# Kernel optimization log

Hardware: AMD Instinct MI355X
Metric: run time of the kernel (lower is better)

The kernel has to match this reference:

```python
import jax, jax.numpy as jnp
import numpy as np

B, D, E, N = 2048, 4096, 512, 8192
BN_EPS = 1e-5
COS_EPS = 1e-8


def setup_inputs() -> dict:
    key = jax.random.key(0)
    k1, k2, k3, k4, k5 = jax.random.split(key, 5)
    vf = jax.random.normal(k1, (B, D), dtype=jnp.float32)
    p_wfs = jax.random.normal(k2, (B, D), dtype=jnp.float32)
    n_wfs = jax.random.normal(k3, (N, E), dtype=jnp.float32)
    # BatchNorm1d(4096) affine params (default init gamma=1, beta=0; use random-ish gamma for generality)
    gamma = jnp.ones((D,), dtype=jnp.float32)
    beta = jnp.zeros((D,), dtype=jnp.float32)
    # Linear(D -> E)
    lim = 1.0 / np.sqrt(D)
    W = jax.random.uniform(k4, (E, D), dtype=jnp.float32, minval=-lim, maxval=lim)
    b = jax.random.uniform(k5, (E,), dtype=jnp.float32, minval=-lim, maxval=lim)
    return {"vf": vf, "p_wfs": p_wfs, "n_wfs": n_wfs, "gamma": gamma, "beta": beta, "W": W, "b": b}


def _row_normalize(x, eps=COS_EPS):
    nrm = jnp.sqrt(jnp.sum(x * x, axis=-1, keepdims=True))
    return x / jnp.maximum(nrm, eps)


def reference(vf, p_wfs, n_wfs, gamma, beta, W, b):
    # BatchNorm1d in training mode: batch mean / biased variance over the batch dim
    mean = jnp.mean(vf, axis=0)
    var = jnp.mean((vf - mean) ** 2, axis=0)
    vfn = (vf - mean) * (gamma / jnp.sqrt(var + BN_EPS)) + beta  # [B, D]

    # Linear + ReLU embedding
    emb = jax.nn.relu(vfn @ W.T + b)  # [B, E]

    # p_e: row-wise cosine(normed vf, p_wfs) -> [B]
    p_e = jnp.sum(_row_normalize(vfn) * _row_normalize(p_wfs), axis=-1)

    # n_e: cosine(emb[v], n_wfs[n]) for all v,n -> one normalized GEMM [B, N]
    n_e = _row_normalize(emb) @ _row_normalize(n_wfs).T

    n_neg = n_wfs.shape[0]
    n_e_stack = n_e.reshape(-1, 1)                      # [B*N, 1]
    p_e_stack = jnp.repeat(p_e, n_neg).reshape(-1, 1)   # [B*N, 1], p_e[v] repeated N times
    return (n_e_stack, p_e_stack)
```

## Files before the change

### kernel.cpp

```cpp
#include <hip/hip_runtime.h>
#include <stdint.h>
#include <stddef.h>

#define B_ 2048
#define D_ 4096
#define E_ 512
#define N_ 8192

typedef unsigned short ushort_t;
typedef __attribute__((ext_vector_type(8))) short short8;
typedef __attribute__((ext_vector_type(4))) float floatx4;
typedef __attribute__((ext_vector_type(4))) unsigned short ushort4_t;

__device__ __forceinline__ void async_load16(const void* g, void* l) {
  __builtin_amdgcn_global_load_lds((__attribute__((address_space(1))) void*)(g),
                                   (__attribute__((address_space(3))) void*)(l), 16, 0, 0);
}

__device__ __forceinline__ ushort_t f2bf(float f) {
  unsigned int u = __float_as_uint(f);
  unsigned int r = (u + 0x7fffu + ((u >> 16) & 1u)) >> 16;
  return (ushort_t)r;
}
__device__ __forceinline__ float bf2f(ushort_t h) {
  return __uint_as_float(((unsigned int)h) << 16);
}

__global__ void bn_partial(const float* __restrict__ vf,
                           float* __restrict__ psum, float* __restrict__ psq) {
  int d = blockIdx.x * 256 + threadIdx.x;
  int chunk = blockIdx.y;
  float s = 0.f, q = 0.f;
  int r0 = chunk * 64;
  for (int r = r0; r < r0 + 64; ++r) {
    float v = vf[(size_t)r * D_ + d];
    s += v; q += v * v;
  }
  psum[chunk * D_ + d] = s;
  psq[chunk * D_ + d]  = q;
}

__global__ void bn_finalize(const float* __restrict__ psum, const float* __restrict__ psq,
                            const float* __restrict__ gamma, const float* __restrict__ beta,
                            float* __restrict__ scale, float* __restrict__ shift) {
  int d = blockIdx.x * 256 + threadIdx.x;
  float s = 0.f, q = 0.f;
  for (int c = 0; c < 32; ++c) { s += psum[c * D_ + d]; q += psq[c * D_ + d]; }
  float mean = s * (1.0f / B_);
  float var  = q * (1.0f / B_) - mean * mean;
  float sc = gamma[d] * rsqrtf(var + 1e-5f);
  scale[d] = sc;
  shift[d] = beta[d] - mean * sc;
}

__global__ void pe_kernel(const float* __restrict__ vf, const float* __restrict__ p,
                          const float* __restrict__ scale, const float* __restrict__ shift,
                          float* __restrict__ pe) {
  int v = blockIdx.x;
  const floatx4* vf4 = (const floatx4*)(vf + (size_t)v * D_);
  const floatx4* p4  = (const floatx4*)(p  + (size_t)v * D_);
  const floatx4* sc4 = (const floatx4*)scale;
  const floatx4* sh4 = (const floatx4*)shift;
  float sd = 0.f, sa = 0.f, sb = 0.f;
  for (int i = threadIdx.x; i < D_ / 4; i += 256) {
    floatx4 x = vf4[i], y = p4[i], s = sc4[i], t = sh4[i];
#pragma unroll
    for (int j = 0; j < 4; ++j) {
      float xn = x[j] * s[j] + t[j];
      sd += xn * y[j]; sa += xn * xn; sb += y[j] * y[j];
    }
  }
  for (int off = 32; off; off >>= 1) {
    sd += __shfl_down(sd, off); sa += __shfl_down(sa, off); sb += __shfl_down(sb, off);
  }
  __shared__ float red[3][4];
  int w = threadIdx.x >> 6, l = threadIdx.x & 63;
  if (l == 0) { red[0][w] = sd; red[1][w] = sa; red[2][w] = sb; }
  __syncthreads();
  if (threadIdx.x == 0) {
    sd = red[0][0] + red[0][1] + red[0][2] + red[0][3];
    sa = red[1][0] + red[1][1] + red[1][2] + red[1][3];
    sb = red[2][0] + red[2][1] + red[2][2] + red[2][3];
    float na = fmaxf(sqrtf(sa), 1e-8f), nb = fmaxf(sqrtf(sb), 1e-8f);
    pe[v] = sd / (na * nb);
  }
}

__global__ void cast_vfn(const float* __restrict__ vf, const float* __restrict__ scale,
                         const float* __restrict__ shift, ushort_t* __restrict__ out) {
  size_t i = ((size_t)blockIdx.x * 256 + threadIdx.x) * 4;
  int d = (int)(i & (D_ - 1));
  floatx4 x = *(const floatx4*)(vf + i);
  floatx4 s = *(const floatx4*)(scale + d);
  floatx4 t = *(const floatx4*)(shift + d);
  ushort4_t o;
#pragma unroll
  for (int j = 0; j < 4; ++j) o[j] = f2bf(x[j] * s[j] + t[j]);
  *(ushort4_t*)(out + i) = o;
}

__global__ void cast_w(const float* __restrict__ W, ushort_t* __restrict__ out) {
  size_t i = ((size_t)blockIdx.x * 256 + threadIdx.x) * 4;
  floatx4 x = *(const floatx4*)(W + i);
  ushort4_t o;
#pragma unroll
  for (int j = 0; j < 4; ++j) o[j] = f2bf(x[j]);
  *(ushort4_t*)(out + i) = o;
}

__global__ void nw_kernel(const float* __restrict__ nw, ushort_t* __restrict__ nwb,
                          float* __restrict__ inv_nw) {
  int n = blockIdx.x;
  int t = threadIdx.x;
  floatx4 x = ((const floatx4*)(nw + (size_t)n * E_))[t];
  float s = x[0]*x[0] + x[1]*x[1] + x[2]*x[2] + x[3]*x[3];
  ushort4_t o;
#pragma unroll
  for (int j = 0; j < 4; ++j) o[j] = f2bf(x[j]);
  ((ushort4_t*)(nwb + (size_t)n * E_))[t] = o;
  for (int off = 32; off; off >>= 1) s += __shfl_down(s, off);
  __shared__ float r2[2];
  if ((t & 63) == 0) r2[t >> 6] = s;
  __syncthreads();
  if (t == 0) inv_nw[n] = 1.f / fmaxf(sqrtf(r2[0] + r2[1]), 1e-8f);
}

__global__ void emb_norm(const ushort_t* __restrict__ emb, float* __restrict__ inv_emb) {
  int v = blockIdx.x;
  int t = threadIdx.x;
  ushort4_t x = ((const ushort4_t*)(emb + (size_t)v * E_))[t];
  float s = 0.f;
#pragma unroll
  for (int j = 0; j < 4; ++j) { float f = bf2f(x[j]); s += f * f; }
  for (int off = 32; off; off >>= 1) s += __shfl_down(s, off);
  __shared__ float r2[2];
  if ((t & 63) == 0) r2[t >> 6] = s;
  __syncthreads();
  if (t == 0) inv_emb[v] = 1.f / fmaxf(sqrtf(r2[0] + r2[1]), 1e-8f);
}

template <int BM, int BN, int BK, int WROWS, int WCOLS, int MT, int NT>
__device__ __forceinline__ void gemm_core(const ushort_t* __restrict__ A,
                                          const ushort_t* __restrict__ Bt, int K,
                                          int bm0, int bn0,
                                          ushort_t* As, ushort_t* Bs,
                                          floatx4 (&acc)[MT][NT]) {
  const int tid = threadIdx.x, w = tid >> 6, l = tid & 63;
  constexpr int ISS = BM * BK / 2048;
  const int wr = w / WCOLS, wc = w % WCOLS;
  const int m16 = l & 15, q = l >> 4;

  for (int k0 = 0; k0 < K; k0 += BK) {
#pragma unroll
    for (int i = 0; i < ISS; ++i) {
      int e = i * 2048 + tid * 8;
      int row = e / BK, col = e % BK;
      async_load16(A + (size_t)(bm0 + row) * K + (k0 + col), &As[i * 2048 + w * 512]);
    }
#pragma unroll
    for (int i = 0; i < ISS; ++i) {
      int e = i * 2048 + tid * 8;
      int row = e / BK, col = e % BK;
      async_load16(Bt + (size_t)(bn0 + row) * K + (k0 + col), &Bs[i * 2048 + w * 512]);
    }
    __syncthreads();
#pragma unroll
    for (int kc = 0; kc < BK / 32; ++kc) {
      short8 af[MT], bf[NT];
#pragma unroll
      for (int i = 0; i < MT; ++i)
        af[i] = *(const short8*)&As[(wr * (MT * 16) + i * 16 + m16) * BK + kc * 32 + q * 8];
#pragma unroll
      for (int j = 0; j < NT; ++j)
        bf[j] = *(const short8*)&Bs[(wc * (NT * 16) + j * 16 + m16) * BK + kc * 32 + q * 8];
#pragma unroll
      for (int i = 0; i < MT; ++i)
#pragma unroll
        for (int j = 0; j < NT; ++j)
          acc[i][j] = __builtin_amdgcn_mfma_f32_16x16x32_bf16(af[i], bf[j], acc[i][j], 0, 0, 0);
    }
    __syncthreads();
  }
}

__global__ __launch_bounds__(256) void gemm1_kernel(const ushort_t* __restrict__ A,
                                                    const ushort_t* __restrict__ Bt,
                                                    const float* __restrict__ bias,
                                                    ushort_t* __restrict__ C) {
  __shared__ __align__(16) ushort_t As[64 * 128];
  __shared__ __align__(16) ushort_t Bs[64 * 128];
  floatx4 acc[2][2] = {};
  int bm0 = blockIdx.y * 64, bn0 = blockIdx.x * 64;
  gemm_core<64, 64, 128, 2, 2, 2, 2>(A, Bt, D_, bm0, bn0, As, Bs, acc);
  int tid = threadIdx.x, w = tid >> 6, l = tid & 63, m16 = l & 15, q = l >> 4;
  int wr = w >> 1, wc = w & 1;
#pragma unroll
  for (int i = 0; i < 2; ++i)
#pragma unroll
    for (int j = 0; j < 2; ++j) {
      int col = bn0 + wc * 32 + j * 16 + m16;
      float bb = bias[col];
#pragma unroll
      for (int r = 0; r < 4; ++r) {
        int row = bm0 + wr * 32 + i * 16 + q * 4 + r;
        float v = fmaxf(acc[i][j][r] + bb, 0.f);
        C[(size_t)row * E_ + col] = f2bf(v);
      }
    }
}

__global__ __launch_bounds__(256) void gemm2_kernel(const ushort_t* __restrict__ A,
                                                    const ushort_t* __restrict__ Bt,
                                                    const float* __restrict__ inv_a,
                                                    const float* __restrict__ inv_b,
                                                    float* __restrict__ out) {
  __shared__ __align__(16) ushort_t As[128 * 64];
  __shared__ __align__(16) ushort_t Bs[128 * 64];
  floatx4 acc[4][4] = {};
  int bm0 = blockIdx.y * 128, bn0 = blockIdx.x * 128;
  gemm_core<128, 128, 64, 2, 2, 4, 4>(A, Bt, E_, bm0, bn0, As, Bs, acc);
  int tid = threadIdx.x, w = tid >> 6, l = tid & 63, m16 = l & 15, q = l >> 4;
  int wr = w >> 1, wc = w & 1;
#pragma unroll
  for (int i = 0; i < 4; ++i)
#pragma unroll
    for (int j = 0; j < 4; ++j) {
      int col = bn0 + wc * 64 + j * 16 + m16;
      float ib = inv_b[col];
#pragma unroll
      for (int r = 0; r < 4; ++r) {
        int row = bm0 + wr * 64 + i * 16 + q * 4 + r;
        out[(size_t)row * N_ + col] = acc[i][j][r] * inv_a[row] * ib;
      }
    }
}

__global__ void fill_pe(const float* __restrict__ pe, float* __restrict__ out2) {
  size_t i = (size_t)blockIdx.x * 256 + threadIdx.x;
  int v = (int)(i >> 11);
  float p = pe[v];
  floatx4 o = {p, p, p, p};
  ((floatx4*)out2)[i] = o;
}

extern "C" void kernel_launch(void* const* d_in, const int* in_sizes, int n_in,
                              void* d_out, int out_size, void* d_ws, size_t ws_size,
                              hipStream_t stream) {
  (void)in_sizes; (void)n_in; (void)out_size; (void)ws_size;
  const float* vf    = (const float*)d_in[0];
  const float* p_wfs = (const float*)d_in[1];
  const float* n_wfs = (const float*)d_in[2];
  const float* gamma = (const float*)d_in[3];
  const float* beta  = (const float*)d_in[4];
  const float* W     = (const float*)d_in[5];
  const float* bias  = (const float*)d_in[6];
  float* out = (float*)d_out;

  char* ws = (char*)d_ws;
  float* psum    = (float*)ws;  ws += (size_t)32 * D_ * 4;
  float* psq     = (float*)ws;  ws += (size_t)32 * D_ * 4;
  float* scale   = (float*)ws;  ws += (size_t)D_ * 4;
  float* shift   = (float*)ws;  ws += (size_t)D_ * 4;
  float* pe      = (float*)ws;  ws += (size_t)B_ * 4;
  float* inv_nw  = (float*)ws;  ws += (size_t)N_ * 4;
  float* inv_emb = (float*)ws;  ws += (size_t)B_ * 4;
  ushort_t* vfn  = (ushort_t*)ws;  ws += (size_t)B_ * D_ * 2;
  ushort_t* wb   = (ushort_t*)ws;  ws += (size_t)E_ * D_ * 2;
  ushort_t* nwb  = (ushort_t*)ws;  ws += (size_t)N_ * E_ * 2;
  ushort_t* emb  = (ushort_t*)ws;  ws += (size_t)B_ * E_ * 2;

  bn_partial<<<dim3(D_ / 256, 32), 256, 0, stream>>>(vf, psum, psq);
  bn_finalize<<<D_ / 256, 256, 0, stream>>>(psum, psq, gamma, beta, scale, shift);
  pe_kernel<<<B_, 256, 0, stream>>>(vf, p_wfs, scale, shift, pe);
  cast_vfn<<<(B_ * D_ / 4) / 256, 256, 0, stream>>>(vf, scale, shift, vfn);
  cast_w<<<(E_ * D_ / 4) / 256, 256, 0, stream>>>(W, wb);
  nw_kernel<<<N_, 128, 0, stream>>>(n_wfs, nwb, inv_nw);
  gemm1_kernel<<<dim3(E_ / 64, B_ / 64), 256, 0, stream>>>(vfn, wb, bias, emb);
  emb_norm<<<B_, 128, 0, stream>>>(emb, inv_emb);
  gemm2_kernel<<<dim3(N_ / 128, B_ / 128), 256, 0, stream>>>(emb, nwb, inv_emb, inv_nw, out);
  fill_pe<<<(B_ * N_ / 4) / 256, 256, 0, stream>>>(pe, out + (size_t)B_ * N_);
}
```

Measured before the change: 320.0 us.

## Fuse BN cast into pe kernel, split-K gemm1, fuse pe fill into gemm2

Merges the vfn bf16 cast into the pe cosine kernel so vf is read once. gemm1 becomes a split-K GEMM over 4 K-slices writing fp32 partials, followed by a reduce kernel that applies bias, ReLU, bf16 cast and the row norm, which replaces emb_norm. The p_e broadcast fill moves into the gemm2 epilogue, and the epilogue loop is reordered to hoist inv_a and inv_b loads. This trades extra fp32 partial traffic for more gemm1 parallelism and fewer launches. The fused gemm2 epilogue now issues strided scalar stores for the 64MB broadcast output, where fill_pe used vector stores.

After: 283.6 us. 1.13x faster.

```diff
diff --git a/kernel.cpp b/kernel.cpp
--- a/kernel.cpp
+++ b/kernel.cpp
@@ -6,6 +6,7 @@
 #define D_ 4096
 #define E_ 512
 #define N_ 8192
+#define SPLITK 4
 
 typedef unsigned short ushort_t;
 typedef __attribute__((ext_vector_type(8))) short short8;
@@ -53,22 +54,29 @@
   shift[d] = beta[d] - mean * sc;
 }
 
-__global__ void pe_kernel(const float* __restrict__ vf, const float* __restrict__ p,
-                          const float* __restrict__ scale, const float* __restrict__ shift,
-                          float* __restrict__ pe) {
+__global__ __launch_bounds__(256) void pe_cast(const float* __restrict__ vf,
+                                               const float* __restrict__ p,
+                                               const float* __restrict__ scale,
+                                               const float* __restrict__ shift,
+                                               ushort_t* __restrict__ vfn,
+                                               float* __restrict__ pe) {
   int v = blockIdx.x;
   const floatx4* vf4 = (const floatx4*)(vf + (size_t)v * D_);
   const floatx4* p4  = (const floatx4*)(p  + (size_t)v * D_);
   const floatx4* sc4 = (const floatx4*)scale;
   const floatx4* sh4 = (const floatx4*)shift;
+  ushort_t* vrow = vfn + (size_t)v * D_;
   float sd = 0.f, sa = 0.f, sb = 0.f;
   for (int i = threadIdx.x; i < D_ / 4; i += 256) {
     floatx4 x = vf4[i], y = p4[i], s = sc4[i], t = sh4[i];
+    ushort4_t o;
 #pragma unroll
     for (int j = 0; j < 4; ++j) {
       float xn = x[j] * s[j] + t[j];
+      o[j] = f2bf(xn);
       sd += xn * y[j]; sa += xn * xn; sb += y[j] * y[j];
     }
+    *(ushort4_t*)(vrow + i * 4) = o;
   }
   for (int off = 32; off; off >>= 1) {
     sd += __shfl_down(sd, off); sa += __shfl_down(sa, off); sb += __shfl_down(sb, off);
@@ -86,19 +94,6 @@
   }
 }
 
-__global__ void cast_vfn(const float* __restrict__ vf, const float* __restrict__ scale,
-                         const float* __restrict__ shift, ushort_t* __restrict__ out) {
-  size_t i = ((size_t)blockIdx.x * 256 + threadIdx.x) * 4;
-  int d = (int)(i & (D_ - 1));
-  floatx4 x = *(const floatx4*)(vf + i);
-  floatx4 s = *(const floatx4*)(scale + d);
-  floatx4 t = *(const floatx4*)(shift + d);
-  ushort4_t o;
-#pragma unroll
-  for (int j = 0; j < 4; ++j) o[j] = f2bf(x[j] * s[j] + t[j]);
-  *(ushort4_t*)(out + i) = o;
-}
-
 __global__ void cast_w(const float* __restrict__ W, ushort_t* __restrict__ out) {
   size_t i = ((size_t)blockIdx.x * 256 + threadIdx.x) * 4;
   floatx4 x = *(const floatx4*)(W + i);
@@ -125,24 +120,10 @@
   if (t == 0) inv_nw[n] = 1.f / fmaxf(sqrtf(r2[0] + r2[1]), 1e-8f);
 }
 
-__global__ void emb_norm(const ushort_t* __restrict__ emb, float* __restrict__ inv_emb) {
-  int v = blockIdx.x;
-  int t = threadIdx.x;
-  ushort4_t x = ((const ushort4_t*)(emb + (size_t)v * E_))[t];
-  float s = 0.f;
-#pragma unroll
-  for (int j = 0; j < 4; ++j) { float f = bf2f(x[j]); s += f * f; }
-  for (int off = 32; off; off >>= 1) s += __shfl_down(s, off);
-  __shared__ float r2[2];
-  if ((t & 63) == 0) r2[t >> 6] = s;
-  __syncthreads();
-  if (t == 0) inv_emb[v] = 1.f / fmaxf(sqrtf(r2[0] + r2[1]), 1e-8f);
-}
-
-template <int BM, int BN, int BK, int WROWS, int WCOLS, int MT, int NT>
+template <int BM, int BN, int BK, int WCOLS, int MT, int NT>
 __device__ __forceinline__ void gemm_core(const ushort_t* __restrict__ A,
                                           const ushort_t* __restrict__ Bt, int K,
-                                          int bm0, int bn0,
+                                          int kb, int ke, int bm0, int bn0,
                                           ushort_t* As, ushort_t* Bs,
                                           floatx4 (&acc)[MT][NT]) {
   const int tid = threadIdx.x, w = tid >> 6, l = tid & 63;
@@ -150,7 +131,7 @@
   const int wr = w / WCOLS, wc = w % WCOLS;
   const int m16 = l & 15, q = l >> 4;
 
-  for (int k0 = 0; k0 < K; k0 += BK) {
+  for (int k0 = kb; k0 < ke; k0 += BK) {
 #pragma unroll
     for (int i = 0; i < ISS; ++i) {
       int e = i * 2048 + tid * 8;
@@ -183,64 +164,89 @@
   }
 }
 
-__global__ __launch_bounds__(256) void gemm1_kernel(const ushort_t* __restrict__ A,
+__global__ __launch_bounds__(256) void gemm1_splitk(const ushort_t* __restrict__ A,
                                                     const ushort_t* __restrict__ Bt,
-                                                    const float* __restrict__ bias,
-                                                    ushort_t* __restrict__ C) {
-  __shared__ __align__(16) ushort_t As[64 * 128];
-  __shared__ __align__(16) ushort_t Bs[64 * 128];
+                                                    float* __restrict__ partial) {
+  __shared__ __align__(16) ushort_t As[64 * 64];
+  __shared__ __align__(16) ushort_t Bs[64 * 64];
   floatx4 acc[2][2] = {};
-  int bm0 = blockIdx.y * 64, bn0 = blockIdx.x * 64;
-  gemm_core<64, 64, 128, 2, 2, 2, 2>(A, Bt, D_, bm0, bn0, As, Bs, acc);
+  int bm0 = blockIdx.y * 64, bn0 = blockIdx.x * 64, s = blockIdx.z;
+  int kb = s * (D_ / SPLITK);
+  gemm_core<64, 64, 64, 2, 2, 2>(A, Bt, D_, kb, kb + D_ / SPLITK, bm0, bn0, As, Bs, acc);
   int tid = threadIdx.x, w = tid >> 6, l = tid & 63, m16 = l & 15, q = l >> 4;
   int wr = w >> 1, wc = w & 1;
+  float* out = partial + (size_t)s * B_ * E_;
 #pragma unroll
   for (int i = 0; i < 2; ++i)
 #pragma unroll
     for (int j = 0; j < 2; ++j) {
       int col = bn0 + wc * 32 + j * 16 + m16;
-      float bb = bias[col];
 #pragma unroll
       for (int r = 0; r < 4; ++r) {
         int row = bm0 + wr * 32 + i * 16 + q * 4 + r;
-        float v = fmaxf(acc[i][j][r] + bb, 0.f);
-        C[(size_t)row * E_ + col] = f2bf(v);
+        out[(size_t)row * E_ + col] = acc[i][j][r];
       }
     }
+}
+
+__global__ __launch_bounds__(128) void gemm1_reduce(const float* __restrict__ partial,
+                                                    const float* __restrict__ bias,
+                                                    ushort_t* __restrict__ emb,
+                                                    float* __restrict__ inv_emb) {
+  int row = blockIdx.x, t = threadIdx.x;
+  floatx4 v = {0.f, 0.f, 0.f, 0.f};
+#pragma unroll
+  for (int s = 0; s < SPLITK; ++s)
+    v += *(const floatx4*)&partial[(size_t)s * B_ * E_ + (size_t)row * E_ + t * 4];
+  floatx4 bb = *(const floatx4*)&bias[t * 4];
+  ushort4_t o;
+  float sumsq = 0.f;
+#pragma unroll
+  for (int j = 0; j < 4; ++j) {
+    float f = fmaxf(v[j] + bb[j], 0.f);
+    o[j] = f2bf(f);
+    float fb = bf2f(o[j]);
+    sumsq += fb * fb;
+  }
+  *(ushort4_t*)(emb + (size_t)row * E_ + t * 4) = o;
+  for (int off = 32; off; off >>= 1) sumsq += __shfl_down(sumsq, off);
+  __shared__ float r2[2];
+  if ((t & 63) == 0) r2[t >> 6] = sumsq;
+  __syncthreads();
+  if (t == 0) inv_emb[row] = 1.f / fmaxf(sqrtf(r2[0] + r2[1]), 1e-8f);
 }
 
 __global__ __launch_bounds__(256) void gemm2_kernel(const ushort_t* __restrict__ A,
                                                     const ushort_t* __restrict__ Bt,
                                                     const float* __restrict__ inv_a,
                                                     const float* __restrict__ inv_b,
+                                                    const float* __restrict__ pe,
                                                     float* __restrict__ out) {
   __shared__ __align__(16) ushort_t As[128 * 64];
   __shared__ __align__(16) ushort_t Bs[128 * 64];
   floatx4 acc[4][4] = {};
   int bm0 = blockIdx.y * 128, bn0 = blockIdx.x * 128;
-  gemm_core<128, 128, 64, 2, 2, 4, 4>(A, Bt, E_, bm0, bn0, As, Bs, acc);
+  gemm_core<128, 128, 64, 2, 4, 4>(A, Bt, E_, 0, E_, bm0, bn0, As, Bs, acc);
   int tid = threadIdx.x, w = tid >> 6, l = tid & 63, m16 = l & 15, q = l >> 4;
   int wr = w >> 1, wc = w & 1;
+  float* out2 = out + (size_t)B_ * N_;
+  float ibv[4];
+#pragma unroll
+  for (int j = 0; j < 4; ++j) ibv[j] = inv_b[bn0 + wc * 64 + j * 16 + m16];
 #pragma unroll
   for (int i = 0; i < 4; ++i)
 #pragma unroll
-    for (int j = 0; j < 4; ++j) {
-      int col = bn0 + wc * 64 + j * 16 + m16;
-      float ib = inv_b[col];
-#pragma unroll
-      for (int r = 0; r < 4; ++r) {
-        int row = bm0 + wr * 64 + i * 16 + q * 4 + r;
-        out[(size_t)row * N_ + col] = acc[i][j][r] * inv_a[row] * ib;
+    for (int r = 0; r < 4; ++r) {
+      int row = bm0 + wr * 64 + i * 16 + q * 4 + r;
+      float ia = inv_a[row];
+      float pv = pe[row];
+      size_t base = (size_t)row * N_ + bn0 + wc * 64 + m16;
+#pragma unroll
+      for (int j = 0; j < 4; ++j) {
+        out[base + j * 16]  = acc[i][j][r] * ia * ibv[j];
+        out2[base + j * 16] = pv;
       }
     }
-}
-
-__global__ void fill_pe(const float* __restrict__ pe, float* __restrict__ out2) {
-  size_t i = (size_t)blockIdx.x * 256 + threadIdx.x;
-  int v = (int)(i >> 11);
-  float p = pe[v];
-  floatx4 o = {p, p, p, p};
-  ((floatx4*)out2)[i] = o;
 }
 
 extern "C" void kernel_launch(void* const* d_in, const int* in_sizes, int n_in,
@@ -264,6 +270,7 @@
   float* pe      = (float*)ws;  ws += (size_t)B_ * 4;
   float* inv_nw  = (float*)ws;  ws += (size_t)N_ * 4;
   float* inv_emb = (float*)ws;  ws += (size_t)B_ * 4;
+  float* partial = (float*)ws;  ws += (size_t)SPLITK * B_ * E_ * 4;
   ushort_t* vfn  = (ushort_t*)ws;  ws += (size_t)B_ * D_ * 2;
   ushort_t* wb   = (ushort_t*)ws;  ws += (size_t)E_ * D_ * 2;
   ushort_t* nwb  = (ushort_t*)ws;  ws += (size_t)N_ * E_ * 2;
@@ -271,12 +278,10 @@
 
   bn_partial<<<dim3(D_ / 256, 32), 256, 0, stream>>>(vf, psum, psq);
   bn_finalize<<<D_ / 256, 256, 0, stream>>>(psum, psq, gamma, beta, scale, shift);
-  pe_kernel<<<B_, 256, 0, stream>>>(vf, p_wfs, scale, shift, pe);
-  cast_vfn<<<(B_ * D_ / 4) / 256, 256, 0, stream>>>(vf, scale, shift, vfn);
+  pe_cast<<<B_, 256, 0, stream>>>(vf, p_wfs, scale, shift, vfn, pe);
   cast_w<<<(E_ * D_ / 4) / 256, 256, 0, stream>>>(W, wb);
   nw_kernel<<<N_, 128, 0, stream>>>(n_wfs, nwb, inv_nw);
-  gemm1_kernel<<<dim3(E_ / 64, B_ / 64), 256, 0, stream>>>(vfn, wb, bias, emb);
-  emb_norm<<<B_, 128, 0, stream>>>(emb, inv_emb);
-  gemm2_kernel<<<dim3(N_ / 128, B_ / 128), 256, 0, stream>>>(emb, nwb, inv_emb, inv_nw, out);
-  fill_pe<<<(B_ * N_ / 4) / 256, 256, 0, stream>>>(pe, out + (size_t)B_ * N_);
-}
+  gemm1_splitk<<<dim3(E_ / 64, B_ / 64, SPLITK), 256, 0, stream>>>(vfn, wb, partial);
+  gemm1_reduce<<<B_, 128, 0, stream>>>(partial, bias, emb, inv_emb);
+  gemm2_kernel<<<dim3(N_ / 128, B_ / 128), 256, 0, stream>>>(emb, nwb, inv_emb, inv_nw, pe, out);
+}
```
